# Kernel optimization log

Hardware: AMD Instinct MI355X
Metric: run time of the kernel (lower is better)

## Reference

```python
import jax, jax.numpy as jnp
import numpy as np

B, T, C = 2, 2048, 2048
H, HD = 16, 128  # num_heads, head_dim; inner_dim = H*HD = C
EPS = 1e-8


def _hadamard(n):
    # Sylvester construction, orthonormal scaling 1/sqrt(n)
    h = np.array([[1.0]], dtype=np.float32)
    while h.shape[0] < n:
        h = np.block([[h, h], [h, -h]])
    return jnp.asarray(h / np.sqrt(n), dtype=jnp.float32)


def _round_ste(x):
    # straight-through rounding (matches int8 training-time quantization semantics)
    return x + jax.lax.stop_gradient(jnp.round(x) - x)


def q8_linear(x, w):
    # dynamic per-token int8 activation quant + per-out-channel int8 weight quant
    s_x = jnp.max(jnp.abs(x), axis=-1, keepdims=True) / 127.0 + EPS   # (B,T,1)
    xq = _round_ste(jnp.clip(x / s_x, -127.0, 127.0))
    s_w = jnp.max(jnp.abs(w), axis=-1, keepdims=True) / 127.0 + EPS   # (O,1)
    wq = _round_ste(jnp.clip(w / s_w, -127.0, 127.0))
    return jnp.einsum('btk,ok->bto', xq, wq) * s_x * s_w[:, 0]


def rmsnorm(x, g, eps=1e-6):
    return x * jax.lax.rsqrt(jnp.mean(x * x, axis=-1, keepdims=True) + eps) * g


def apply_rope(x, cos, sin):
    # x: (B,T,H*HD); cos/sin: (T,HD/2); interleaved rotary per head
    b, t, c = x.shape
    xh = x.reshape(b, t, -1, HD)
    x1, x2 = xh[..., 0::2], xh[..., 1::2]
    co = cos[None, :, None, :]
    si = sin[None, :, None, :]
    o1 = x1 * co - x2 * si
    o2 = x1 * si + x2 * co
    out = jnp.stack([o1, o2], axis=-1).reshape(b, t, -1, HD)
    return out.reshape(b, t, c)


def setup_inputs() -> dict:
    key = jax.random.key(0)
    ks = jax.random.split(key, 8)
    hidden_states = jax.random.normal(ks[0], (B, T, C), jnp.float32)
    attention_mask = jax.random.randint(ks[1], (B,), 1, T + 1).astype(jnp.int32)  # valid lengths
    sc = 1.0 / np.sqrt(C)
    wq = jax.random.normal(ks[2], (H * HD, C), jnp.float32) * sc
    wk = jax.random.normal(ks[3], (H * HD, C), jnp.float32) * sc
    wv = jax.random.normal(ks[4], (H * HD, C), jnp.float32) * sc
    wo = jax.random.normal(ks[5], (C, H * HD), jnp.float32) * (1.0 / np.sqrt(H * HD))
    q_gamma = jnp.ones((H * HD,), jnp.float32)
    k_gamma = jnp.ones((H * HD,), jnp.float32)
    inv_freq = 1.0 / (10000.0 ** (np.arange(0, HD, 2, dtype=np.float32) / HD))
    freqs = np.outer(np.arange(T, dtype=np.float32), inv_freq)  # (T, HD/2)
    cos = jnp.asarray(np.cos(freqs), jnp.float32)
    sin = jnp.asarray(np.sin(freqs), jnp.float32)
    return {"hidden_states": hidden_states, "attention_mask": attention_mask,
            "wq": wq, "wk": wk, "wv": wv, "wo": wo,
            "q_gamma": q_gamma, "k_gamma": k_gamma, "cos": cos, "sin": sin}


def reference(hidden_states, attention_mask, wq, wk, wv, wo, q_gamma, k_gamma, cos, sin):
    b, t, c = hidden_states.shape
    q = rmsnorm(q8_linear(hidden_states, wq), q_gamma)
    k = rmsnorm(q8_linear(hidden_states, wk), k_gamma)
    v = q8_linear(hidden_states, wv)
    q = apply_rope(q, cos, sin)
    k = apply_rope(k, cos, sin)
    # (B,T,H*HD) -> (B,H,T,HD)
    q = q.reshape(b, t, H, HD).transpose(0, 2, 1, 3)
    k = k.reshape(b, t, H, HD).transpose(0, 2, 1, 3)
    v = v.reshape(b, t, H, HD).transpose(0, 2, 1, 3)
    # Hadamard rotation of q/k head dims (orthonormal -> preserves qk dot products)
    Hm = _hadamard(HD)
    qh = q @ Hm
    kh = k @ Hm
    scores = jnp.einsum('bhqd,bhkd->bhqk', qh, kh) * (1.0 / np.sqrt(HD))
    # ragged batch mask: keys beyond per-batch valid length are masked out
    valid = jnp.arange(t)[None, :] < attention_mask[:, None]   # (B,T)
    scores = jnp.where(valid[:, None, None, :], scores, -1e9)
    p = jax.nn.softmax(scores, axis=-1)
    o = jnp.einsum('bhqk,bhkd->bhqd', p, v)
    o = o.transpose(0, 2, 1, 3).reshape(b, t, c)
    return q8_linear(o, wo)
```

## Files before the change

kernel.cpp:

```cpp
#include <hip/hip_runtime.h>
#include <stdint.h>

typedef unsigned short u16;
typedef unsigned int u32;
typedef int v4i __attribute__((ext_vector_type(4)));
typedef float v4f __attribute__((ext_vector_type(4)));
typedef short v8s __attribute__((ext_vector_type(8)));

#define Bn 2
#define Tn 2048
#define Cn 2048
#define Hn 16
#define HDn 128

__device__ __forceinline__ float b2f(u16 u) {
    u32 x = ((u32)u) << 16;
    float f;
    __builtin_memcpy(&f, &x, 4);
    return f;
}
__device__ __forceinline__ u16 f2b(float f) {
    u32 x;
    __builtin_memcpy(&x, &f, 4);
    u32 r = (x + 0x7fffu + ((x >> 16) & 1u)) >> 16;
    return (u16)r;
}

__device__ __forceinline__ void async16(const void* g, void* l) {
    __builtin_amdgcn_global_load_lds(
        (const __attribute__((address_space(1))) u32*)g,
        (__attribute__((address_space(3))) u32*)l, 16, 0, 0);
}

__global__ __launch_bounds__(256) void quant_all(
    const float* __restrict__ w0, const float* __restrict__ w1,
    const float* __restrict__ w2, const float* __restrict__ w3,
    const float* __restrict__ hid, int8_t* __restrict__ Q,
    float* __restrict__ S) {
    int r = blockIdx.x;
    const float* src;
    int ro;
    if (r < 2048) { src = w0; ro = r; }
    else if (r < 4096) { src = w1; ro = r - 2048; }
    else if (r < 6144) { src = w2; ro = r - 4096; }
    else if (r < 8192) { src = w3; ro = r - 6144; }
    else { src = hid; ro = r - 8192; }
    const float* x = src + (size_t)ro * Cn;
    int tid = threadIdx.x;
    float4 v0 = ((const float4*)x)[tid * 2];
    float4 v1 = ((const float4*)x)[tid * 2 + 1];
    float a[8] = {v0.x, v0.y, v0.z, v0.w, v1.x, v1.y, v1.z, v1.w};
    float m = 0.f;
#pragma unroll
    for (int i = 0; i < 8; i++) m = fmaxf(m, fabsf(a[i]));
#pragma unroll
    for (int o = 32; o; o >>= 1) m = fmaxf(m, __shfl_xor(m, o));
    __shared__ float sm[4];
    if ((tid & 63) == 0) sm[tid >> 6] = m;
    __syncthreads();
    m = fmaxf(fmaxf(sm[0], sm[1]), fmaxf(sm[2], sm[3]));
    float s = m * (1.0f / 127.0f) + 1e-8f;
    if (tid == 0) S[r] = s;
    u32 lo = 0, hi = 0;
#pragma unroll
    for (int i = 0; i < 8; i++) {
        float q = rintf(fminf(127.f, fmaxf(-127.f, a[i] / s)));
        int qi = (int)q;
        u32 byte = (u32)(qi & 0xff);
        if (i < 4) lo |= byte << (8 * i);
        else hi |= byte << (8 * (i - 4));
    }
    u32* qp = (u32*)(Q + (size_t)r * Cn);
    qp[tid * 2] = lo;
    qp[tid * 2 + 1] = hi;
}

__global__ __launch_bounds__(256) void quant_rows(const float* __restrict__ X,
                                                  int8_t* __restrict__ Q,
                                                  float* __restrict__ S) {
    int r = blockIdx.x;
    const float* x = X + (size_t)r * Cn;
    int tid = threadIdx.x;
    float4 v0 = ((const float4*)x)[tid * 2];
    float4 v1 = ((const float4*)x)[tid * 2 + 1];
    float a[8] = {v0.x, v0.y, v0.z, v0.w, v1.x, v1.y, v1.z, v1.w};
    float m = 0.f;
#pragma unroll
    for (int i = 0; i < 8; i++) m = fmaxf(m, fabsf(a[i]));
#pragma unroll
    for (int o = 32; o; o >>= 1) m = fmaxf(m, __shfl_xor(m, o));
    __shared__ float sm[4];
    if ((tid & 63) == 0) sm[tid >> 6] = m;
    __syncthreads();
    m = fmaxf(fmaxf(sm[0], sm[1]), fmaxf(sm[2], sm[3]));
    float s = m * (1.0f / 127.0f) + 1e-8f;
    if (tid == 0) S[r] = s;
    u32 lo = 0, hi = 0;
#pragma unroll
    for (int i = 0; i < 8; i++) {
        float q = rintf(fminf(127.f, fmaxf(-127.f, a[i] / s)));
        int qi = (int)q;
        u32 byte = (u32)(qi & 0xff);
        if (i < 4) lo |= byte << (8 * i);
        else hi |= byte << (8 * (i - 4));
    }
    u32* qp = (u32*)(Q + (size_t)r * Cn);
    qp[tid * 2] = lo;
    qp[tid * 2 + 1] = hi;
}

__global__ __launch_bounds__(256) void gemm_i8(
    const int8_t* __restrict__ A, const int8_t* __restrict__ Bw,
    const float* __restrict__ sA, const float* __restrict__ sB,
    void* __restrict__ Co, long long bStride, long long sbStride,
    long long cStride, int fp32out) {
    int z = blockIdx.z;
    Bw += (size_t)z * bStride;
    sB += (size_t)z * sbStride;
    const int K = 2048, N = 2048;
    __shared__ int8_t As[128 * 64];
    __shared__ int8_t Bs[128 * 64];
    int m0 = blockIdx.x * 128, n0 = blockIdx.y * 128;
    int tid = threadIdx.x, w = tid >> 6, lane = tid & 63;
    int quad = lane >> 4, l15 = lane & 15;
    int wy = w >> 1, wx = w & 1;
    const v4i zi = {0, 0, 0, 0};
    v4i acc[4][4];
#pragma unroll
    for (int i = 0; i < 4; i++)
#pragma unroll
        for (int j = 0; j < 4; j++) acc[i][j] = zi;
    int lrow = lane >> 2;
    int slot = lane & 3;
    int srow = w * 32 + lrow;
    int klog = ((slot ^ (lrow & 3)) * 16);
    const int8_t* ga = A + (size_t)(m0 + srow) * K + klog;
    const int8_t* gb = Bw + (size_t)(n0 + srow) * K + klog;
    int8_t* la = &As[srow * 64 + slot * 16];
    int8_t* lb = &Bs[srow * 64 + slot * 16];
    for (int k0 = 0; k0 < K; k0 += 64) {
        async16(ga + k0, la);
        async16(ga + k0 + (size_t)16 * K, la + 16 * 64);
        async16(gb + k0, lb);
        async16(gb + k0 + (size_t)16 * K, lb + 16 * 64);
        __syncthreads();
        int swz = (quad ^ (l15 & 3)) * 16;
        v4i af[4], bf4[4];
#pragma unroll
        for (int i = 0; i < 4; i++)
            af[i] = *(const v4i*)&As[(wy * 64 + i * 16 + l15) * 64 + swz];
#pragma unroll
        for (int j = 0; j < 4; j++)
            bf4[j] = *(const v4i*)&Bs[(wx * 64 + j * 16 + l15) * 64 + swz];
#pragma unroll
        for (int i = 0; i < 4; i++)
#pragma unroll
            for (int j = 0; j < 4; j++)
                acc[i][j] = __builtin_amdgcn_mfma_i32_16x16x64_i8(
                    af[i], bf4[j], acc[i][j], 0, 0, 0);
        __syncthreads();
    }
#pragma unroll
    for (int i = 0; i < 4; i++) {
        int mb = m0 + wy * 64 + i * 16 + quad * 4;
        float s0 = sA[mb], s1 = sA[mb + 1], s2 = sA[mb + 2], s3 = sA[mb + 3];
#pragma unroll
        for (int j = 0; j < 4; j++) {
            int n = n0 + wx * 64 + j * 16 + l15;
            float sb = sB[n];
            if (fp32out) {
                float* cp = (float*)Co + (size_t)cStride * z + (size_t)mb * N + n;
                cp[0] = (float)acc[i][j][0] * s0 * sb;
                cp[N] = (float)acc[i][j][1] * s1 * sb;
                cp[2 * N] = (float)acc[i][j][2] * s2 * sb;
                cp[3 * N] = (float)acc[i][j][3] * s3 * sb;
            } else {
                u16* cp = (u16*)Co + (size_t)cStride * z + (size_t)mb * N + n;
                cp[0] = f2b((float)acc[i][j][0] * s0 * sb);
                cp[N] = f2b((float)acc[i][j][1] * s1 * sb);
                cp[2 * N] = f2b((float)acc[i][j][2] * s2 * sb);
                cp[3 * N] = f2b((float)acc[i][j][3] * s3 * sb);
            }
        }
    }
}

__global__ __launch_bounds__(256) void norm_rope2(u16* __restrict__ Qb,
                                                  u16* __restrict__ Kb,
                                                  const float* __restrict__ qg,
                                                  const float* __restrict__ kg,
                                                  const float* __restrict__ cs,
                                                  const float* __restrict__ sn) {
    int row = blockIdx.x;
    int isq = row < 4096;
    row &= 4095;
    u16* x = (isq ? Qb : Kb) + (size_t)row * Cn;
    const float* g = isq ? qg : kg;
    float ps = isq ? 0.08838834764831845f : 1.0f;
    int t = row & (Tn - 1);
    int tid = threadIdx.x;
    uint4 raw = ((const uint4*)x)[tid];
    u16 us[8];
    us[0] = raw.x & 0xffff; us[1] = raw.x >> 16;
    us[2] = raw.y & 0xffff; us[3] = raw.y >> 16;
    us[4] = raw.z & 0xffff; us[5] = raw.z >> 16;
    us[6] = raw.w & 0xffff; us[7] = raw.w >> 16;
    float v[8];
#pragma unroll
    for (int i = 0; i < 8; i++) v[i] = b2f(us[i]);
    float ss = 0.f;
#pragma unroll
    for (int i = 0; i < 8; i++) ss += v[i] * v[i];
#pragma unroll
    for (int o = 32; o; o >>= 1) ss += __shfl_xor(ss, o);
    __shared__ float sm[4];
    if ((tid & 63) == 0) sm[tid >> 6] = ss;
    __syncthreads();
    ss = sm[0] + sm[1] + sm[2] + sm[3];
    float r = rsqrtf(ss * (1.f / 2048.f) + 1e-6f) * ps;
    float4 g0 = ((const float4*)g)[tid * 2];
    float4 g1 = ((const float4*)g)[tid * 2 + 1];
    float n[8];
    n[0] = v[0] * r * g0.x; n[1] = v[1] * r * g0.y;
    n[2] = v[2] * r * g0.z; n[3] = v[3] * r * g0.w;
    n[4] = v[4] * r * g1.x; n[5] = v[5] * r * g1.y;
    n[6] = v[6] * r * g1.z; n[7] = v[7] * r * g1.w;
    int pi = (tid & 15) * 4;
    float4 c4 = *(const float4*)(cs + t * 64 + pi);
    float4 s4 = *(const float4*)(sn + t * 64 + pi);
    float o[8];
    o[0] = n[0] * c4.x - n[1] * s4.x; o[1] = n[0] * s4.x + n[1] * c4.x;
    o[2] = n[2] * c4.y - n[3] * s4.y; o[3] = n[2] * s4.y + n[3] * c4.y;
    o[4] = n[4] * c4.z - n[5] * s4.z; o[5] = n[4] * s4.z + n[5] * c4.z;
    o[6] = n[6] * c4.w - n[7] * s4.w; o[7] = n[6] * s4.w + n[7] * c4.w;
    uint4 out;
    out.x = (u32)f2b(o[0]) | ((u32)f2b(o[1]) << 16);
    out.y = (u32)f2b(o[2]) | ((u32)f2b(o[3]) << 16);
    out.z = (u32)f2b(o[4]) | ((u32)f2b(o[5]) << 16);
    out.w = (u32)f2b(o[6]) | ((u32)f2b(o[7]) << 16);
    ((uint4*)x)[tid] = out;
}

__global__ __launch_bounds__(256) void vtrans(const u16* __restrict__ V,
                                              u16* __restrict__ Vt) {
    int bh = blockIdx.y;
    int b = bh >> 4, h = bh & 15;
    int t0 = blockIdx.x * 64;
    __shared__ u32 tile[64][133];
    int tid = threadIdx.x;
    int r = tid >> 2, seg = (tid & 3) * 32;
    const uint4* src =
        (const uint4*)(V + ((size_t)b * Tn + t0 + r) * Cn + h * HDn + seg);
#pragma unroll
    for (int i = 0; i < 4; i++) {
        uint4 u = src[i];
        u32 uu[4] = {u.x, u.y, u.z, u.w};
#pragma unroll
        for (int j = 0; j < 4; j++) {
            tile[r][seg + i * 8 + j * 2] = uu[j] & 0xffff;
            tile[r][seg + i * 8 + j * 2 + 1] = uu[j] >> 16;
        }
    }
    __syncthreads();
    int d = tid >> 1, tseg = (tid & 1) * 32;
    u16* dst = Vt + ((size_t)bh * HDn + d) * Tn + t0 + tseg;
#pragma unroll
    for (int i = 0; i < 4; i++) {
        u32 p0 = tile[tseg + i * 8 + 0][d] | (tile[tseg + i * 8 + 1][d] << 16);
        u32 p1 = tile[tseg + i * 8 + 2][d] | (tile[tseg + i * 8 + 3][d] << 16);
        u32 p2 = tile[tseg + i * 8 + 4][d] | (tile[tseg + i * 8 + 5][d] << 16);
        u32 p3 = tile[tseg + i * 8 + 6][d] | (tile[tseg + i * 8 + 7][d] << 16);
        ((uint4*)dst)[i] = make_uint4(p0, p1, p2, p3);
    }
}

#define KS_S 136
#define VS_S 72
#define PS_S 72
__global__ __launch_bounds__(256) void flash(const u16* __restrict__ Qb,
                                             const u16* __restrict__ Kb,
                                             const u16* __restrict__ Vt,
                                             const int* __restrict__ mask,
                                             float* __restrict__ O) {
    int qt = blockIdx.x, bh = blockIdx.y;
    int b = bh >> 4, h = bh & 15;
    int L = mask[b];
    int nkfull = L >> 6;
    int nk = (L + 63) >> 6;
    __shared__ u16 Ks[64 * KS_S];
    __shared__ u16 Vs[128 * VS_S];
    __shared__ u16 Ps[4][16 * PS_S];
    int tid = threadIdx.x, w = tid >> 6, lane = tid & 63;
    int quad = lane >> 4, l15 = lane & 15;
    const u16* qrow =
        Qb + ((size_t)b * Tn + qt * 64 + w * 16 + l15) * Cn + h * HDn;
    v8s aq[4];
#pragma unroll
    for (int kk = 0; kk < 4; kk++)
        aq[kk] = *(const v8s*)(qrow + kk * 32 + quad * 8);
    float sum[4] = {0.f, 0.f, 0.f, 0.f};
    const v4f zf = {0.f, 0.f, 0.f, 0.f};
    v4f oacc[8];
#pragma unroll
    for (int i = 0; i < 8; i++) oacc[i] = zf;
    for (int kt = 0; kt < nk; kt++) {
        int kb0 = kt * 64;
        {
            int r = tid >> 2, seg = (tid & 3) * 32;
            const uint4* src = (const uint4*)(Kb + ((size_t)b * Tn + kb0 + r) * Cn +
                                              h * HDn + seg);
            uint4* dst = (uint4*)(Ks + r * KS_S + seg);
#pragma unroll
            for (int i = 0; i < 4; i++) dst[i] = src[i];
        }
        {
            int d = tid >> 1, seg = (tid & 1) * 32;
            const uint4* src =
                (const uint4*)(Vt + ((size_t)bh * HDn + d) * Tn + kb0 + seg);
            uint4* dst = (uint4*)(Vs + d * VS_S + seg);
#pragma unroll
            for (int i = 0; i < 4; i++) dst[i] = src[i];
        }
        __syncthreads();
        v4f sacc[4];
#pragma unroll
        for (int nj = 0; nj < 4; nj++) sacc[nj] = zf;
#pragma unroll
        for (int kk = 0; kk < 4; kk++) {
#pragma unroll
            for (int nj = 0; nj < 4; nj++) {
                v8s bk =
                    *(const v8s*)(Ks + (nj * 16 + l15) * KS_S + kk * 32 + quad * 8);
                sacc[nj] = __builtin_amdgcn_mfma_f32_16x16x32_bf16(aq[kk], bk,
                                                                   sacc[nj], 0, 0, 0);
            }
        }
        u16 pb[4][4];
        if (kt < nkfull) {
#pragma unroll
            for (int nj = 0; nj < 4; nj++)
#pragma unroll
                for (int r2 = 0; r2 < 4; r2++) {
                    float p = __expf(sacc[nj][r2]);
                    sum[r2] += p;
                    pb[nj][r2] = f2b(p);
                }
        } else {
#pragma unroll
            for (int nj = 0; nj < 4; nj++) {
                bool valid = (kb0 + nj * 16 + l15) < L;
#pragma unroll
                for (int r2 = 0; r2 < 4; r2++) {
                    float p = valid ? __expf(sacc[nj][r2]) : 0.f;
                    sum[r2] += p;
                    pb[nj][r2] = f2b(p);
                }
            }
        }
        u16* pw = &Ps[w][0];
#pragma unroll
        for (int nj = 0; nj < 4; nj++)
#pragma unroll
            for (int r2 = 0; r2 < 4; r2++)
                pw[(quad * 4 + r2) * PS_S + nj * 16 + l15] = pb[nj][r2];
        asm volatile("s_waitcnt lgkmcnt(0)" ::: "memory");
#pragma unroll
        for (int kk2 = 0; kk2 < 2; kk2++) {
            v8s ap = *(const v8s*)(pw + l15 * PS_S + kk2 * 32 + quad * 8);
#pragma unroll
            for (int nj2 = 0; nj2 < 8; nj2++) {
                v8s bv =
                    *(const v8s*)(Vs + (nj2 * 16 + l15) * VS_S + kk2 * 32 + quad * 8);
                oacc[nj2] = __builtin_amdgcn_mfma_f32_16x16x32_bf16(ap, bv, oacc[nj2],
                                                                    0, 0, 0);
            }
        }
        __syncthreads();
    }
    float inv4[4];
#pragma unroll
    for (int r2 = 0; r2 < 4; r2++) {
        float s2 = sum[r2];
#pragma unroll
        for (int o = 8; o; o >>= 1) s2 += __shfl_xor(s2, o);
        inv4[r2] = 1.f / s2;
    }
#pragma unroll
    for (int nj2 = 0; nj2 < 8; nj2++) {
        int d = h * HDn + nj2 * 16 + l15;
#pragma unroll
        for (int r2 = 0; r2 < 4; r2++) {
            int q = qt * 64 + w * 16 + quad * 4 + r2;
            O[((size_t)b * Tn + q) * Cn + d] = oacc[nj2][r2] * inv4[r2];
        }
    }
}

extern "C" void kernel_launch(void* const* d_in, const int* in_sizes, int n_in,
                              void* d_out, int out_size, void* d_ws,
                              size_t ws_size, hipStream_t stream) {
    const float* hidden = (const float*)d_in[0];
    const int* mask = (const int*)d_in[1];
    const float* wq = (const float*)d_in[2];
    const float* wk = (const float*)d_in[3];
    const float* wv = (const float*)d_in[4];
    const float* wo = (const float*)d_in[5];
    const float* qg = (const float*)d_in[6];
    const float* kg = (const float*)d_in[7];
    const float* cs = (const float*)d_in[8];
    const float* sn = (const float*)d_in[9];

    char* ws = (char*)d_ws;
    int8_t* q8 = (int8_t*)(ws);
    float* sAll = (float*)(ws + 25165824);
    u16* qb = (u16*)(ws + 25214976);
    u16* kb = (u16*)(ws + 41992192);
    u16* vb = (u16*)(ws + 58769408);
    u16* vt = (u16*)(ws + 75546624);
    float* Obuf = (float*)(ws + 92323840);
    int8_t* hid8 = q8 + 16777216;
    float* sx = sAll + 8192;

    quant_all<<<12288, 256, 0, stream>>>(wq, wk, wv, wo, hidden, q8, sAll);

    gemm_i8<<<dim3(32, 16, 3), 256, 0, stream>>>(hid8, q8, sx, sAll, (void*)qb,
                                                 4194304LL, 2048LL, 8388608LL, 0);

    norm_rope2<<<8192, 256, 0, stream>>>(qb, kb, qg, kg, cs, sn);
    vtrans<<<dim3(32, 32), 256, 0, stream>>>(vb, vt);

    flash<<<dim3(32, 32), 256, 0, stream>>>(qb, kb, vt, mask, Obuf);

    quant_rows<<<4096, 256, 0, stream>>>(Obuf, hid8, sx);
    gemm_i8<<<dim3(32, 16, 1), 256, 0, stream>>>(hid8, q8 + 12582912, sx,
                                                 sAll + 6144, d_out, 0LL, 0LL,
                                                 0LL, 1);
}
```

Before: 356.0 us.

## Repartition flash attention warps by key columns with async swizzled K/V loads

The flash kernel changes its work split. Each warp now holds all 64 query rows of Q in registers and computes scores for its own 16-key slice, then owns 32 output head-dim columns for the PV product, so each K/V fragment loaded from LDS feeds four MFMAs. K and V tiles are brought in with async 16-byte global-to-LDS copies into XOR-swizzled unpadded layouts in place of register-staged copies. The cost is more Q registers, an extra barrier per tile for the shared P buffer, and a cross-warp shared-memory reduction of the softmax denominators.

```diff
diff --git a/kernel.cpp b/kernel.cpp
--- a/kernel.cpp
+++ b/kernel.cpp
@@ -274,126 +274,148 @@
     }
 }
 
-#define KS_S 136
-#define VS_S 72
-#define PS_S 72
-__global__ __launch_bounds__(256) void flash(const u16* __restrict__ Qb,
-                                             const u16* __restrict__ Kb,
-                                             const u16* __restrict__ Vt,
-                                             const int* __restrict__ mask,
-                                             float* __restrict__ O) {
+__global__ __launch_bounds__(256, 3) void flash(const u16* __restrict__ Qb,
+                                                const u16* __restrict__ Kb,
+                                                const u16* __restrict__ Vt,
+                                                const int* __restrict__ mask,
+                                                float* __restrict__ O) {
     int qt = blockIdx.x, bh = blockIdx.y;
     int b = bh >> 4, h = bh & 15;
     int L = mask[b];
     int nkfull = L >> 6;
     int nk = (L + 63) >> 6;
-    __shared__ u16 Ks[64 * KS_S];
-    __shared__ u16 Vs[128 * VS_S];
-    __shared__ u16 Ps[4][16 * PS_S];
+    __shared__ u16 Ks[64 * 128];
+    __shared__ u16 Vs[128 * 64];
+    __shared__ u16 Ps[64 * 72];
+    __shared__ float sred[256];
+    __shared__ float sinv[64];
     int tid = threadIdx.x, w = tid >> 6, lane = tid & 63;
     int quad = lane >> 4, l15 = lane & 15;
-    const u16* qrow =
-        Qb + ((size_t)b * Tn + qt * 64 + w * 16 + l15) * Cn + h * HDn;
-    v8s aq[4];
-#pragma unroll
-    for (int kk = 0; kk < 4; kk++)
-        aq[kk] = *(const v8s*)(qrow + kk * 32 + quad * 8);
-    float sum[4] = {0.f, 0.f, 0.f, 0.f};
+
+    v8s aq[4][4];
+#pragma unroll
+    for (int i = 0; i < 4; i++)
+#pragma unroll
+        for (int kk = 0; kk < 4; kk++)
+            aq[i][kk] = *(const v8s*)(Qb +
+                                      ((size_t)b * Tn + qt * 64 + i * 16 + l15) * Cn +
+                                      h * HDn + kk * 32 + quad * 8);
+
+    const u16* ksp[4];
+    u16* kdp[4];
+    const u16* vsp[4];
+    u16* vdp[4];
+#pragma unroll
+    for (int cc = 0; cc < 4; cc++) {
+        int c = w * 4 + cc;
+        int rk = c * 4 + (lane >> 4);
+        int sk = lane & 15;
+        int lgk = sk ^ (rk & 7);
+        ksp[cc] = Kb + ((size_t)b * Tn + rk) * Cn + h * HDn + lgk * 8;
+        kdp[cc] = Ks + rk * 128 + sk * 8;
+        int rv = c * 8 + (lane >> 3);
+        int sv = lane & 7;
+        int lgv = sv ^ (rv & 7);
+        vsp[cc] = Vt + ((size_t)bh * HDn + rv) * Tn + lgv * 8;
+        vdp[cc] = Vs + rv * 64 + sv * 8;
+    }
+
+    float sum16[16];
+#pragma unroll
+    for (int j = 0; j < 16; j++) sum16[j] = 0.f;
     const v4f zf = {0.f, 0.f, 0.f, 0.f};
-    v4f oacc[8];
-#pragma unroll
-    for (int i = 0; i < 8; i++) oacc[i] = zf;
+    v4f oacc[4][2];
+#pragma unroll
+    for (int m = 0; m < 4; m++) {
+        oacc[m][0] = zf;
+        oacc[m][1] = zf;
+    }
+    int swz = ((l15 & 7) ^ quad) << 3;
+
     for (int kt = 0; kt < nk; kt++) {
-        int kb0 = kt * 64;
-        {
-            int r = tid >> 2, seg = (tid & 3) * 32;
-            const uint4* src = (const uint4*)(Kb + ((size_t)b * Tn + kb0 + r) * Cn +
-                                              h * HDn + seg);
-            uint4* dst = (uint4*)(Ks + r * KS_S + seg);
-#pragma unroll
-            for (int i = 0; i < 4; i++) dst[i] = src[i];
-        }
-        {
-            int d = tid >> 1, seg = (tid & 1) * 32;
-            const uint4* src =
-                (const uint4*)(Vt + ((size_t)bh * HDn + d) * Tn + kb0 + seg);
-            uint4* dst = (uint4*)(Vs + d * VS_S + seg);
-#pragma unroll
-            for (int i = 0; i < 4; i++) dst[i] = src[i];
-        }
         __syncthreads();
-        v4f sacc[4];
-#pragma unroll
-        for (int nj = 0; nj < 4; nj++) sacc[nj] = zf;
+#pragma unroll
+        for (int cc = 0; cc < 4; cc++) async16(ksp[cc], kdp[cc]);
+#pragma unroll
+        for (int cc = 0; cc < 4; cc++) async16(vsp[cc], vdp[cc]);
+#pragma unroll
+        for (int cc = 0; cc < 4; cc++) {
+            ksp[cc] += 64 * Cn;
+            vsp[cc] += 64;
+        }
+        __syncthreads();
+        v4f sacc[4] = {zf, zf, zf, zf};
+        const u16* krow = Ks + (w * 16 + l15) * 128;
 #pragma unroll
         for (int kk = 0; kk < 4; kk++) {
-#pragma unroll
-            for (int nj = 0; nj < 4; nj++) {
-                v8s bk =
-                    *(const v8s*)(Ks + (nj * 16 + l15) * KS_S + kk * 32 + quad * 8);
-                sacc[nj] = __builtin_amdgcn_mfma_f32_16x16x32_bf16(aq[kk], bk,
-                                                                   sacc[nj], 0, 0, 0);
+            v8s bk = *(const v8s*)(krow + ((((kk * 4 + quad) ^ (l15 & 7))) << 3));
+#pragma unroll
+            for (int i = 0; i < 4; i++)
+                sacc[i] = __builtin_amdgcn_mfma_f32_16x16x32_bf16(aq[i][kk], bk,
+                                                                  sacc[i], 0, 0, 0);
+        }
+        bool valid = (kt < nkfull) || ((kt * 64 + w * 16 + l15) < L);
+#pragma unroll
+        for (int i = 0; i < 4; i++)
+#pragma unroll
+            for (int r2 = 0; r2 < 4; r2++) {
+                float p = valid ? __expf(sacc[i][r2]) : 0.f;
+                sum16[i * 4 + r2] += p;
+                Ps[(i * 16 + quad * 4 + r2) * 72 + w * 16 + l15] = f2b(p);
             }
-        }
-        u16 pb[4][4];
-        if (kt < nkfull) {
-#pragma unroll
-            for (int nj = 0; nj < 4; nj++)
-#pragma unroll
-                for (int r2 = 0; r2 < 4; r2++) {
-                    float p = __expf(sacc[nj][r2]);
-                    sum[r2] += p;
-                    pb[nj][r2] = f2b(p);
-                }
-        } else {
-#pragma unroll
-            for (int nj = 0; nj < 4; nj++) {
-                bool valid = (kb0 + nj * 16 + l15) < L;
-#pragma unroll
-                for (int r2 = 0; r2 < 4; r2++) {
-                    float p = valid ? __expf(sacc[nj][r2]) : 0.f;
-                    sum[r2] += p;
-                    pb[nj][r2] = f2b(p);
-                }
+        __syncthreads();
+#pragma unroll
+        for (int kk2 = 0; kk2 < 2; kk2++) {
+            v8s ap[4];
+#pragma unroll
+            for (int m = 0; m < 4; m++)
+                ap[m] = *(const v8s*)(Ps + (m * 16 + l15) * 72 + kk2 * 32 + quad * 8);
+#pragma unroll
+            for (int nbi = 0; nbi < 2; nbi++) {
+                int vr = (2 * w + nbi) * 16 + l15;
+                v8s bv = *(const v8s*)(Vs + vr * 64 +
+                                       ((((kk2 * 4 + quad) ^ (l15 & 7))) << 3));
+#pragma unroll
+                for (int m = 0; m < 4; m++)
+                    oacc[m][nbi] = __builtin_amdgcn_mfma_f32_16x16x32_bf16(
+                        ap[m], bv, oacc[m][nbi], 0, 0, 0);
             }
         }
-        u16* pw = &Ps[w][0];
-#pragma unroll
-        for (int nj = 0; nj < 4; nj++)
+    }
+#pragma unroll
+    for (int j = 0; j < 16; j++) {
+        float s = sum16[j];
+        s += __shfl_xor(s, 1);
+        s += __shfl_xor(s, 2);
+        s += __shfl_xor(s, 4);
+        s += __shfl_xor(s, 8);
+        sum16[j] = s;
+    }
+    if (l15 == 0) {
+#pragma unroll
+        for (int i = 0; i < 4; i++)
 #pragma unroll
             for (int r2 = 0; r2 < 4; r2++)
-                pw[(quad * 4 + r2) * PS_S + nj * 16 + l15] = pb[nj][r2];
-        asm volatile("s_waitcnt lgkmcnt(0)" ::: "memory");
-#pragma unroll
-        for (int kk2 = 0; kk2 < 2; kk2++) {
-            v8s ap = *(const v8s*)(pw + l15 * PS_S + kk2 * 32 + quad * 8);
-#pragma unroll
-            for (int nj2 = 0; nj2 < 8; nj2++) {
-                v8s bv =
-                    *(const v8s*)(Vs + (nj2 * 16 + l15) * VS_S + kk2 * 32 + quad * 8);
-                oacc[nj2] = __builtin_amdgcn_mfma_f32_16x16x32_bf16(ap, bv, oacc[nj2],
-                                                                    0, 0, 0);
+                sred[w * 64 + i * 16 + quad * 4 + r2] = sum16[i * 4 + r2];
+    }
+    __syncthreads();
+    if (tid < 64)
+        sinv[tid] =
+            1.f / (sred[tid] + sred[64 + tid] + sred[128 + tid] + sred[192 + tid]);
+    __syncthreads();
+#pragma unroll
+    for (int m = 0; m < 4; m++)
+#pragma unroll
+        for (int r2 = 0; r2 < 4; r2++) {
+            float inv = sinv[m * 16 + quad * 4 + r2];
+            int row = qt * 64 + m * 16 + quad * 4 + r2;
+#pragma unroll
+            for (int nbi = 0; nbi < 2; nbi++) {
+                int d = h * HDn + (2 * w + nbi) * 16 + l15;
+                O[((size_t)b * Tn + row) * Cn + d] = oacc[m][nbi][r2] * inv;
             }
         }
-        __syncthreads();
-    }
-    float inv4[4];
-#pragma unroll
-    for (int r2 = 0; r2 < 4; r2++) {
-        float s2 = sum[r2];
-#pragma unroll
-        for (int o = 8; o; o >>= 1) s2 += __shfl_xor(s2, o);
-        inv4[r2] = 1.f / s2;
-    }
-#pragma unroll
-    for (int nj2 = 0; nj2 < 8; nj2++) {
-        int d = h * HDn + nj2 * 16 + l15;
-#pragma unroll
-        for (int r2 = 0; r2 < 4; r2++) {
-            int q = qt * 64 + w * 16 + quad * 4 + r2;
-            O[((size_t)b * Tn + q) * Cn + d] = oacc[nj2][r2] * inv4[r2];
-        }
-    }
+    (void)swz;
 }
 
 extern "C" void kernel_launch(void* const* d_in, const int* in_sizes, int n_in,
```

New measurement: 351.7 us. No clear change (-1.2%).
